# Performance work log

Measured on AMD Instinct MI355X. Metric: run time of the kernel, lower is better.

The kernel has to match this reference:

```python
import jax, jax.numpy as jnp
import numpy as np

H = 2048
NH = 16
DH = H // NH
EPS = 1e-05


def setup_inputs() -> dict:
    key = jax.random.key(0)
    ks = jax.random.split(key, 12)
    B, S, A = 4, 2048, 512
    s = 1.0 / np.sqrt(H)
    inp = {
        "hidden_states": jax.random.normal(ks[0], (B, S, H), jnp.float32),
        "audio_tokens": jax.random.normal(ks[1], (B, A, H), jnp.float32),
        "attention_mask": jax.random.randint(ks[2], (B, A), 0, 2).astype(jnp.float32),
        "Wq": jax.random.normal(ks[3], (H, H), jnp.float32) * s,
        "bq": jnp.zeros((H,), jnp.float32),
        "Wk": jax.random.normal(ks[4], (H, H), jnp.float32) * s,
        "bk": jnp.zeros((H,), jnp.float32),
        "Wv": jax.random.normal(ks[5], (H, H), jnp.float32) * s,
        "bv": jnp.zeros((H,), jnp.float32),
        "Wo": jax.random.normal(ks[6], (H, H), jnp.float32) * s,
        "bo": jnp.zeros((H,), jnp.float32),
        "gamma": jnp.ones((H,), jnp.float32),
        "beta": jnp.zeros((H,), jnp.float32),
    }
    return inp


def reference(hidden_states, audio_tokens, attention_mask,
              Wq, bq, Wk, bk, Wv, bv, Wo, bo, gamma, beta):
    B, S, _ = hidden_states.shape
    A = audio_tokens.shape[1]
    # projections (weights stored [in, out])
    q = (hidden_states @ Wq + bq).reshape(B, S, NH, DH)
    k = (audio_tokens @ Wk + bk).reshape(B, A, NH, DH)
    v = (audio_tokens @ Wv + bv).reshape(B, A, NH, DH)
    # scores: [B, NH, S, A]
    scores = jnp.einsum('bqhd,bkhd->bhqk', q, k) / np.sqrt(DH)
    scores = scores + attention_mask[:, None, None, :] * -10000.0
    probs = jax.nn.softmax(scores, axis=-1)
    # context: [B, S, NH, DH] -> [B, S, H]
    ctx = jnp.einsum('bhqk,bkhd->bqhd', probs, v).reshape(B, S, H)
    out = ctx @ Wo + bo
    # residual + LayerNorm
    x = out + hidden_states
    mu = jnp.mean(x, axis=-1, keepdims=True)
    var = jnp.mean(jnp.square(x - mu), axis=-1, keepdims=True)
    return (x - mu) * jax.lax.rsqrt(var + EPS) * gamma + beta
```

## Files before the change

### kernel.cpp

```cpp
#include <hip/hip_runtime.h>

#define HDIM 2048
#define NHEAD 16
#define DHEAD 128
#define BATCH 4
#define SEQ 2048
#define AUD 512

typedef unsigned short u16;
typedef unsigned int u32;
typedef __bf16 bf16_t;
typedef bf16_t bf16x8 __attribute__((ext_vector_type(8)));
typedef short short8 __attribute__((ext_vector_type(8)));
typedef float f32x4 __attribute__((ext_vector_type(4)));

typedef const __attribute__((address_space(1))) u32 gas_u32;
typedef __attribute__((address_space(3))) u32 las_u32;

__device__ __forceinline__ float b2f(u16 h) {
  union { u32 u; float f; } v; v.u = ((u32)h) << 16; return v.f;
}
__device__ __forceinline__ u16 f2b(float f) {
  union { float f; u32 u; } v; v.f = f;
  u32 r = (v.u + 0x7FFFu + ((v.u >> 16) & 1u)) >> 16;
  return (u16)r;
}

__global__ __launch_bounds__(256) void cvt2_k(const float* __restrict__ s0,
                                              u16* __restrict__ d0, int n0,
                                              const float* __restrict__ s1,
                                              u16* __restrict__ d1, int n1) {
  int i = blockIdx.x * 256 + threadIdx.x;
  const float* src; u16* dst; int j;
  if (i < n0) { src = s0; dst = d0; j = i; }
  else { j = i - n0; if (j >= n1) return; src = s1; dst = d1; }
  const float4* s4 = (const float4*)src;
  float4 a = s4[2 * j], b = s4[2 * j + 1];
  short8 o;
  o[0] = (short)f2b(a.x); o[1] = (short)f2b(a.y);
  o[2] = (short)f2b(a.z); o[3] = (short)f2b(a.w);
  o[4] = (short)f2b(b.x); o[5] = (short)f2b(b.y);
  o[6] = (short)f2b(b.z); o[7] = (short)f2b(b.w);
  *(short8*)(dst + (size_t)j * 8) = o;
}

__global__ __launch_bounds__(256) void transpose4_k(
    const float* __restrict__ Wq, const float* __restrict__ Wk,
    const float* __restrict__ Wv, const float* __restrict__ Wo,
    u16* __restrict__ dst4) {
  const float* src = (blockIdx.z == 0) ? Wq
                   : (blockIdx.z == 1) ? Wk
                   : (blockIdx.z == 2) ? Wv : Wo;
  u16* dst = dst4 + (size_t)blockIdx.z * HDIM * HDIM;
  __shared__ float tile[32][33];
  int tx = threadIdx.x, ty = threadIdx.y;
  int x = blockIdx.x * 32 + tx;
  int y0 = blockIdx.y * 32;
#pragma unroll
  for (int j = 0; j < 32; j += 8)
    tile[ty + j][tx] = src[(size_t)(y0 + ty + j) * HDIM + x];
  __syncthreads();
  int x2 = y0 + tx;
  int y2 = blockIdx.x * 32;
#pragma unroll
  for (int j = 0; j < 32; j += 8)
    dst[(size_t)(y2 + ty + j) * HDIM + x2] = f2b(tile[tx][ty + j]);
}

__global__ __launch_bounds__(256) void gemm_bt(
    const u16* __restrict__ A, int lda,
    const u16* __restrict__ Bt, int ldb,
    void* __restrict__ Cv, int ldc,
    const float* __restrict__ bias, float alpha, int M, int N, int K, int cmode) {
  __shared__ u16 As[128 * 32];
  __shared__ u16 Bs[128 * 32];

  int lane = threadIdx.x & 63;
  int wave = threadIdx.x >> 6;
  int gdx = gridDim.x;
  int id = blockIdx.y * gdx + blockIdx.x;
  int cpx = (gdx * gridDim.y) >> 3;
  int sid = (id & 7) * cpx + (id >> 3);
  int m0 = (sid / gdx) * 128;
  int n0 = (sid % gdx) * 128;
  int wm = (wave & 1) * 64;
  int wn = (wave >> 1) * 64;
  int row16 = lane & 15;
  int quad = lane >> 4;

  int sr = (lane >> 2);
  int sc = (lane & 3) * 8;

  f32x4 acc[4][4];
#pragma unroll
  for (int i = 0; i < 4; i++)
#pragma unroll
    for (int j = 0; j < 4; j++) acc[i][j] = (f32x4){0.f, 0.f, 0.f, 0.f};

  for (int k0 = 0; k0 < K; k0 += 32) {
#pragma unroll
    for (int t = 0; t < 2; t++) {
      int chunk = wave * 2 + t;
      int r = chunk * 16 + sr;
      const u16* ga = A + (size_t)(m0 + r) * lda + k0 + sc;
      const u16* gb = Bt + (size_t)(n0 + r) * ldb + k0 + sc;
      __builtin_amdgcn_global_load_lds((gas_u32*)ga, (las_u32*)(As + chunk * 512), 16, 0, 0);
      __builtin_amdgcn_global_load_lds((gas_u32*)gb, (las_u32*)(Bs + chunk * 512), 16, 0, 0);
    }
    __syncthreads();

    short8 af[4], bf[4];
#pragma unroll
    for (int mt = 0; mt < 4; mt++)
      af[mt] = *(const short8*)(As + (wm + mt * 16 + row16) * 32 + quad * 8);
#pragma unroll
    for (int nt = 0; nt < 4; nt++)
      bf[nt] = *(const short8*)(Bs + (wn + nt * 16 + row16) * 32 + quad * 8);
#pragma unroll
    for (int mt = 0; mt < 4; mt++)
#pragma unroll
      for (int nt = 0; nt < 4; nt++)
        acc[mt][nt] = __builtin_amdgcn_mfma_f32_16x16x32_bf16(
            __builtin_bit_cast(bf16x8, af[mt]), __builtin_bit_cast(bf16x8, bf[nt]),
            acc[mt][nt], 0, 0, 0);
    __syncthreads();
  }

#pragma unroll
  for (int nt = 0; nt < 4; nt++) {
    int nn = n0 + wn + nt * 16 + row16;
    float bv = bias ? bias[nn] : 0.f;
#pragma unroll
    for (int mt = 0; mt < 4; mt++) {
#pragma unroll
      for (int r = 0; r < 4; r++) {
        int mm = m0 + wm + mt * 16 + quad * 4 + r;
        float val = (acc[mt][nt][r] + bv) * alpha;
        if (cmode == 2) {
          ((float*)Cv)[(size_t)mm * ldc + nn] = val;
        } else if (cmode == 1) {
          int bb = mm >> 9, aa = mm & 511;
          int hh = nn >> 7, dd = nn & 127;
          ((u16*)Cv)[((size_t)((bb * 16 + hh) * 128 + dd)) * 512 + aa] = f2b(val);
        } else {
          ((u16*)Cv)[(size_t)mm * ldc + nn] = f2b(val);
        }
      }
    }
  }
}

__global__ __launch_bounds__(512, 2) void gemm_ring8(
    const u16* __restrict__ A, int lda,
    const u16* __restrict__ Bt, int ldb,
    void* __restrict__ Cv, int ldc,
    const float* __restrict__ bias, float alpha, int K, int cmode) {
  __shared__ u16 As[4][256 * 32];
  __shared__ u16 Bs[4][256 * 32];

  int tid = threadIdx.x;
  int lane = tid & 63, wave = tid >> 6;
  int wr = wave >> 2, wc = wave & 3;
  int row16 = lane & 15, quad = lane >> 4;
  int cofs = (quad * 8) ^ (((row16 >> 1) & 3) << 3);

  int gdx = gridDim.x;
  int id = blockIdx.y * gdx + blockIdx.x;
  int cpx = (gdx * gridDim.y) >> 3;
  int sid = (id & 7) * cpx + (id >> 3);
  int n0 = (sid % gdx) * 256;
  int m0 = (sid / gdx) * 256;

  int r0 = tid >> 2;
  int c0 = ((tid & 3) ^ ((r0 >> 1) & 3)) * 8;

  f32x4 acc[8][4];
#pragma unroll
  for (int i = 0; i < 8; i++)
#pragma unroll
    for (int j = 0; j < 4; j++) acc[i][j] = (f32x4){0.f, 0.f, 0.f, 0.f};

  auto stageA = [&](int slot, int k0) {
#pragma unroll
    for (int l = 0; l < 2; l++) {
      int row = l * 128 + r0;
      __builtin_amdgcn_global_load_lds(
          (gas_u32*)(A + (size_t)(m0 + row) * lda + k0 + c0),
          (las_u32*)(&As[slot][(l * 512 + tid) * 8]), 16, 0, 0);
    }
  };
  auto stageB = [&](int slot, int k0) {
#pragma unroll
    for (int l = 0; l < 2; l++) {
      int row = l * 128 + r0;
      __builtin_amdgcn_global_load_lds(
          (gas_u32*)(Bt + (size_t)(n0 + row) * ldb + k0 + c0),
          (las_u32*)(&Bs[slot][(l * 512 + tid) * 8]), 16, 0, 0);
    }
  };

  int NT = K >> 5;
  stageA(0, 0);  stageB(0, 0);
  stageA(1, 32); stageB(1, 32);
  stageA(2, 64); stageB(2, 64);
  asm volatile("s_waitcnt vmcnt(8)" ::: "memory");
  __builtin_amdgcn_s_barrier();

  for (int kt = 0; kt < NT; ++kt) {
    int slot = kt & 3;
    int sp = (kt + 3) & 3;
    bool pf = (kt + 3) < NT;
    const u16* as = &As[slot][0];
    const u16* bs = &Bs[slot][0];

    short8 bfr[4], af[4];
#pragma unroll
    for (int ni = 0; ni < 4; ni++)
      bfr[ni] = *(const short8*)(bs + (wc * 64 + ni * 16 + row16) * 32 + cofs);
#pragma unroll
    for (int mi = 0; mi < 4; mi++)
      af[mi] = *(const short8*)(as + (wr * 128 + mi * 16 + row16) * 32 + cofs);
    if (pf) stageA(sp, (kt + 3) << 5);
    __builtin_amdgcn_s_barrier();
    asm volatile("s_waitcnt lgkmcnt(0)" ::: "memory");
    __builtin_amdgcn_s_setprio(1);
#pragma unroll
    for (int mi = 0; mi < 4; mi++)
#pragma unroll
      for (int ni = 0; ni < 4; ni++)
        acc[mi][ni] = __builtin_amdgcn_mfma_f32_16x16x32_bf16(
            __builtin_bit_cast(bf16x8, af[mi]), __builtin_bit_cast(bf16x8, bfr[ni]),
            acc[mi][ni], 0, 0, 0);
    __builtin_amdgcn_s_setprio(0);
    __builtin_amdgcn_s_barrier();

    short8 ag[4];
#pragma unroll
    for (int mi = 0; mi < 4; mi++)
      ag[mi] = *(const short8*)(as + (wr * 128 + (mi + 4) * 16 + row16) * 32 + cofs);
    if (pf) stageB(sp, (kt + 3) << 5);
    {
      int nf = NT - 2 - kt;
      if (nf >= 2)      asm volatile("s_waitcnt vmcnt(8)" ::: "memory");
      else if (nf == 1) asm volatile("s_waitcnt vmcnt(4)" ::: "memory");
      else              asm volatile("s_waitcnt vmcnt(0)" ::: "memory");
    }
    __builtin_amdgcn_s_barrier();
    asm volatile("s_waitcnt lgkmcnt(0)" ::: "memory");
    __builtin_amdgcn_s_setprio(1);
#pragma unroll
    for (int mi = 0; mi < 4; mi++)
#pragma unroll
      for (int ni = 0; ni < 4; ni++)
        acc[mi + 4][ni] = __builtin_amdgcn_mfma_f32_16x16x32_bf16(
            __builtin_bit_cast(bf16x8, ag[mi]), __builtin_bit_cast(bf16x8, bfr[ni]),
            acc[mi + 4][ni], 0, 0, 0);
    __builtin_amdgcn_s_setprio(0);
    __builtin_amdgcn_s_barrier();
  }

#pragma unroll
  for (int ni = 0; ni < 4; ni++) {
    int nn = n0 + wc * 64 + ni * 16 + row16;
    float bv = bias ? bias[nn] : 0.f;
#pragma unroll
    for (int mi = 0; mi < 8; mi++) {
#pragma unroll
      for (int r = 0; r < 4; r++) {
        int mm = m0 + wr * 128 + mi * 16 + quad * 4 + r;
        float val = (acc[mi][ni][r] + bv) * alpha;
        if (cmode == 2) ((float*)Cv)[(size_t)mm * ldc + nn] = val;
        else            ((u16*)Cv)[(size_t)mm * ldc + nn] = f2b(val);
      }
    }
  }
}

__global__ __launch_bounds__(256) void flash_k(
    const u16* __restrict__ Q, const u16* __restrict__ K,
    const u16* __restrict__ Vt, const float* __restrict__ mask,
    u16* __restrict__ Ctx) {
  __shared__ u16 KP[128 * 128];
  __shared__ u16 Vs[128 * 128];

  int bh = blockIdx.y, b = bh >> 4, h = bh & 15;
  int q0 = blockIdx.x * 128;
  int lane = threadIdx.x & 63, wave = threadIdx.x >> 6;
  int row16 = lane & 15, quad = lane >> 4;
  int wq = wave * 32;
  int swr = (row16 & 7) << 3;

  const u16* qbase = Q + ((size_t)(b * SEQ + q0)) * HDIM + h * DHEAD;
  const u16* kbase = K + ((size_t)b * AUD) * HDIM + h * DHEAD;
  const u16* vbase = Vt + ((size_t)(b * NHEAD + h)) * DHEAD * AUD;
  const float* mp = mask + b * AUD;

  short8 qf[2][4];
#pragma unroll
  for (int mt = 0; mt < 2; mt++)
#pragma unroll
    for (int ks = 0; ks < 4; ks++)
      qf[mt][ks] = *(const short8*)(qbase + (size_t)(wq + mt * 16 + row16) * HDIM +
                                    ks * 32 + quad * 8);

  f32x4 oacc[2][8];
  float lacc[2][4];
#pragma unroll
  for (int mt = 0; mt < 2; mt++) {
#pragma unroll
    for (int nt = 0; nt < 8; nt++) oacc[mt][nt] = (f32x4){0.f, 0.f, 0.f, 0.f};
#pragma unroll
    for (int r = 0; r < 4; r++) lacc[mt][r] = 0.f;
  }

  int sl = (lane >> 4);
  int scol = (lane & 15) * 8;

  for (int kt = 0; kt < 4; kt++) {
#pragma unroll
    for (int t = 0; t < 8; t++) {
      int c = wave * 8 + t;
      int r = c * 4 + sl;
      int csw = scol ^ ((r & 7) << 3);
      __builtin_amdgcn_global_load_lds(
          (gas_u32*)(kbase + (size_t)(kt * 128 + r) * HDIM + csw),
          (las_u32*)(KP + c * 512), 16, 0, 0);
      __builtin_amdgcn_global_load_lds(
          (gas_u32*)(vbase + (size_t)r * AUD + kt * 128 + csw),
          (las_u32*)(Vs + c * 512), 16, 0, 0);
    }
    __syncthreads();

    f32x4 sacc[2][8];
#pragma unroll
    for (int mt = 0; mt < 2; mt++)
#pragma unroll
      for (int nt = 0; nt < 8; nt++) sacc[mt][nt] = (f32x4){0.f, 0.f, 0.f, 0.f};
#pragma unroll
    for (int ks = 0; ks < 4; ks++) {
      short8 bf[8];
      int cofs = (ks * 32 + quad * 8) ^ swr;
#pragma unroll
      for (int nt = 0; nt < 8; nt++)
        bf[nt] = *(const short8*)(KP + (nt * 16 + row16) * 128 + cofs);
      __builtin_amdgcn_s_setprio(1);
#pragma unroll
      for (int mt = 0; mt < 2; mt++)
#pragma unroll
        for (int nt = 0; nt < 8; nt++)
          sacc[mt][nt] = __builtin_amdgcn_mfma_f32_16x16x32_bf16(
              __builtin_bit_cast(bf16x8, qf[mt][ks]), __builtin_bit_cast(bf16x8, bf[nt]),
              sacc[mt][nt], 0, 0, 0);
      __builtin_amdgcn_s_setprio(0);
    }

#pragma unroll
    for (int nt = 0; nt < 8; nt++) {
      float mval = mp[kt * 128 + nt * 16 + row16] * (-10000.0f);
#pragma unroll
      for (int mt = 0; mt < 2; mt++)
#pragma unroll
        for (int r = 0; r < 4; r++) {
          float e = __expf(sacc[mt][nt][r] + mval);
          sacc[mt][nt][r] = e;
          lacc[mt][r] += e;
        }
    }
    __syncthreads();

#pragma unroll
    for (int mt = 0; mt < 2; mt++)
#pragma unroll
      for (int nt = 0; nt < 8; nt++)
#pragma unroll
        for (int r = 0; r < 4; r++) {
          int prow = wq + mt * 16 + quad * 4 + r;
          KP[prow * 128 + ((nt * 16 + row16) ^ ((prow & 7) << 3))] =
              f2b(sacc[mt][nt][r]);
        }
    __syncthreads();

#pragma unroll
    for (int ks = 0; ks < 4; ks++) {
      short8 af[2], bf[8];
      int cofs = (ks * 32 + quad * 8) ^ swr;
#pragma unroll
      for (int mt = 0; mt < 2; mt++)
        af[mt] = *(const short8*)(KP + (wq + mt * 16 + row16) * 128 + cofs);
#pragma unroll
      for (int nt = 0; nt < 8; nt++)
        bf[nt] = *(const short8*)(Vs + (nt * 16 + row16) * 128 + cofs);
      __builtin_amdgcn_s_setprio(1);
#pragma unroll
      for (int mt = 0; mt < 2; mt++)
#pragma unroll
        for (int nt = 0; nt < 8; nt++)
          oacc[mt][nt] = __builtin_amdgcn_mfma_f32_16x16x32_bf16(
              __builtin_bit_cast(bf16x8, af[mt]), __builtin_bit_cast(bf16x8, bf[nt]),
              oacc[mt][nt], 0, 0, 0);
      __builtin_amdgcn_s_setprio(0);
    }
    __syncthreads();
  }

#pragma unroll
  for (int mt = 0; mt < 2; mt++)
#pragma unroll
    for (int r = 0; r < 4; r++) {
      float s = lacc[mt][r];
      for (int off = 1; off < 16; off <<= 1) s += __shfl_xor(s, off, 64);
      lacc[mt][r] = 1.0f / s;
    }

  u16* cb = Ctx + ((size_t)(b * SEQ + q0 + wq)) * HDIM + h * DHEAD;
#pragma unroll
  for (int mt = 0; mt < 2; mt++)
#pragma unroll
    for (int nt = 0; nt < 8; nt++)
#pragma unroll
      for (int r = 0; r < 4; r++)
        cb[(size_t)(mt * 16 + quad * 4 + r) * HDIM + nt * 16 + row16] =
            f2b(oacc[mt][nt][r] * lacc[mt][r]);
}

__global__ __launch_bounds__(256) void ln_k(const float* O,
                                            const float* __restrict__ hs,
                                            const float* __restrict__ gamma,
                                            const float* __restrict__ beta,
                                            float* out) {
  size_t rowoff = (size_t)blockIdx.x * HDIM;
  float x[8], sum = 0.f, sq = 0.f;
#pragma unroll
  for (int i = 0; i < 8; i++) {
    int idx = threadIdx.x + 256 * i;
    float v = O[rowoff + idx] + hs[rowoff + idx];
    x[i] = v;
    sum += v;
    sq += v * v;
  }
  for (int off = 32; off; off >>= 1) {
    sum += __shfl_xor(sum, off, 64);
    sq += __shfl_xor(sq, off, 64);
  }
  __shared__ float red[8];
  int wave = threadIdx.x >> 6, lane = threadIdx.x & 63;
  if (lane == 0) { red[wave] = sum; red[4 + wave] = sq; }
  __syncthreads();
  sum = red[0] + red[1] + red[2] + red[3];
  sq = red[4] + red[5] + red[6] + red[7];
  float mu = sum * (1.0f / HDIM);
  float var = sq * (1.0f / HDIM) - mu * mu;
  float inv = rsqrtf(var + 1e-5f);
#pragma unroll
  for (int i = 0; i < 8; i++) {
    int idx = threadIdx.x + 256 * i;
    out[rowoff + idx] = (x[i] - mu) * inv * gamma[idx] + beta[idx];
  }
}

extern "C" void kernel_launch(void* const* d_in, const int* in_sizes, int n_in,
                              void* d_out, int out_size, void* d_ws, size_t ws_size,
                              hipStream_t stream) {
  (void)in_sizes; (void)n_in; (void)out_size; (void)ws_size;
  const float* hs   = (const float*)d_in[0];
  const float* at   = (const float*)d_in[1];
  const float* mask = (const float*)d_in[2];
  const float* Wq = (const float*)d_in[3];  const float* bq = (const float*)d_in[4];
  const float* Wk = (const float*)d_in[5];  const float* bk = (const float*)d_in[6];
  const float* Wv = (const float*)d_in[7];  const float* bv = (const float*)d_in[8];
  const float* Wo = (const float*)d_in[9];  const float* bo = (const float*)d_in[10];
  const float* gamma = (const float*)d_in[11];
  const float* beta  = (const float*)d_in[12];
  float* out = (float*)d_out;
  u16* ws = (u16*)d_ws;

  u16* hsb = ws;
  u16* atb = ws + 16777216;
  u16* wT4 = ws + 20971520;
  u16* Q   = ws + 37748736;
  u16* Kb  = ws + 54525952;
  u16* Vt  = ws + 58720256;
  u16* Ctx = ws + 62914560;
  u16* wTq = wT4;
  u16* wTk = wT4 + 4194304;
  u16* wTv = wT4 + 8388608;
  u16* wTo = wT4 + 12582912;

  cvt2_k<<<10240, 256, 0, stream>>>(hs, hsb, 2097152, at, atb, 524288);
  transpose4_k<<<dim3(64, 64, 4), dim3(32, 8), 0, stream>>>(Wq, Wk, Wv, Wo, wT4);

  const float qscale = 0.08838834764831845f;

  gemm_ring8<<<dim3(8, 32), 512, 0, stream>>>(hsb, HDIM, wTq, HDIM, Q, HDIM,
                                              bq, qscale, 2048, 0);
  gemm_bt<<<dim3(16, 16), 256, 0, stream>>>(atb, HDIM, wTk, HDIM, Kb, HDIM,
                                            bk, 1.0f, 2048, 2048, 2048, 0);
  gemm_bt<<<dim3(16, 16), 256, 0, stream>>>(atb, HDIM, wTv, HDIM, Vt, HDIM,
                                            bv, 1.0f, 2048, 2048, 2048, 1);

  flash_k<<<dim3(SEQ / 128, BATCH * NHEAD), 256, 0, stream>>>(Q, Kb, Vt, mask, Ctx);

  gemm_ring8<<<dim3(8, 32), 512, 0, stream>>>(Ctx, HDIM, wTo, HDIM, out, HDIM,
                                              bo, 1.0f, 2048, 2);
  ln_k<<<8192, 256, 0, stream>>>(out, hs, gamma, beta, out);
}
```

Measured before the change: 594.4 us.

## Prefetch next K/V tile into registers during the PV MFMA phase

The first K/V tile is now loaded into LDS before the loop. Each later tile is read from global memory into registers while the P·V MFMAs run, then written into the swizzled LDS buffers after a barrier, which hides global-load latency behind compute. `__syncthreads` is replaced by explicit lgkmcnt waits plus `s_barrier`, and the `s_setprio` hints around the MFMA blocks are removed. The trade-off is 64 extra VGPRs per lane for the prefetch buffers, which may lower occupancy, and the prefetched K/V data now takes a register round trip instead of a direct global-to-LDS load.

```diff
diff --git a/kernel.cpp b/kernel.cpp
--- a/kernel.cpp
+++ b/kernel.cpp
@@ -316,21 +316,21 @@
   int sl = (lane >> 4);
   int scol = (lane & 15) * 8;
 
+#pragma unroll
+  for (int t = 0; t < 8; t++) {
+    int c = wave * 8 + t;
+    int r = c * 4 + sl;
+    int csw = scol ^ ((r & 7) << 3);
+    __builtin_amdgcn_global_load_lds(
+        (gas_u32*)(kbase + (size_t)r * HDIM + csw),
+        (las_u32*)(KP + c * 512), 16, 0, 0);
+    __builtin_amdgcn_global_load_lds(
+        (gas_u32*)(vbase + (size_t)r * AUD + csw),
+        (las_u32*)(Vs + c * 512), 16, 0, 0);
+  }
+  __syncthreads();
+
   for (int kt = 0; kt < 4; kt++) {
-#pragma unroll
-    for (int t = 0; t < 8; t++) {
-      int c = wave * 8 + t;
-      int r = c * 4 + sl;
-      int csw = scol ^ ((r & 7) << 3);
-      __builtin_amdgcn_global_load_lds(
-          (gas_u32*)(kbase + (size_t)(kt * 128 + r) * HDIM + csw),
-          (las_u32*)(KP + c * 512), 16, 0, 0);
-      __builtin_amdgcn_global_load_lds(
-          (gas_u32*)(vbase + (size_t)r * AUD + kt * 128 + csw),
-          (las_u32*)(Vs + c * 512), 16, 0, 0);
-    }
-    __syncthreads();
-
     f32x4 sacc[2][8];
 #pragma unroll
     for (int mt = 0; mt < 2; mt++)
@@ -343,7 +343,6 @@
 #pragma unroll
       for (int nt = 0; nt < 8; nt++)
         bf[nt] = *(const short8*)(KP + (nt * 16 + row16) * 128 + cofs);
-      __builtin_amdgcn_s_setprio(1);
 #pragma unroll
       for (int mt = 0; mt < 2; mt++)
 #pragma unroll
@@ -351,7 +350,6 @@
           sacc[mt][nt] = __builtin_amdgcn_mfma_f32_16x16x32_bf16(
               __builtin_bit_cast(bf16x8, qf[mt][ks]), __builtin_bit_cast(bf16x8, bf[nt]),
               sacc[mt][nt], 0, 0, 0);
-      __builtin_amdgcn_s_setprio(0);
     }
 
 #pragma unroll
@@ -366,7 +364,9 @@
           lacc[mt][r] += e;
         }
     }
-    __syncthreads();
+
+    asm volatile("s_waitcnt lgkmcnt(0)" ::: "memory");
+    __builtin_amdgcn_s_barrier();
 
 #pragma unroll
     for (int mt = 0; mt < 2; mt++)
@@ -378,7 +378,16 @@
           KP[prow * 128 + ((nt * 16 + row16) ^ ((prow & 7) << 3))] =
               f2b(sacc[mt][nt][r]);
         }
-    __syncthreads();
+
+    short8 kreg[8], vreg[8];
+    if (kt < 3) {
+#pragma unroll
+      for (int t = 0; t < 8; t++) {
+        int r = wq + t * 4 + sl;
+        kreg[t] = *(const short8*)(kbase + (size_t)((kt + 1) * 128 + r) * HDIM + scol);
+        vreg[t] = *(const short8*)(vbase + (size_t)r * AUD + (kt + 1) * 128 + scol);
+      }
+    }
 
 #pragma unroll
     for (int ks = 0; ks < 4; ks++) {
@@ -390,7 +399,6 @@
 #pragma unroll
       for (int nt = 0; nt < 8; nt++)
         bf[nt] = *(const short8*)(Vs + (nt * 16 + row16) * 128 + cofs);
-      __builtin_amdgcn_s_setprio(1);
 #pragma unroll
       for (int mt = 0; mt < 2; mt++)
 #pragma unroll
@@ -398,9 +406,23 @@
           oacc[mt][nt] = __builtin_amdgcn_mfma_f32_16x16x32_bf16(
               __builtin_bit_cast(bf16x8, af[mt]), __builtin_bit_cast(bf16x8, bf[nt]),
               oacc[mt][nt], 0, 0, 0);
-      __builtin_amdgcn_s_setprio(0);
-    }
-    __syncthreads();
+    }
+
+    asm volatile("s_waitcnt lgkmcnt(0)" ::: "memory");
+    __builtin_amdgcn_s_barrier();
+
+    if (kt < 3) {
+      asm volatile("s_waitcnt vmcnt(0)" ::: "memory");
+#pragma unroll
+      for (int t = 0; t < 8; t++) {
+        int r = wq + t * 4 + sl;
+        int cs = scol ^ ((r & 7) << 3);
+        *(short8*)(KP + r * 128 + cs) = kreg[t];
+        *(short8*)(Vs + r * 128 + cs) = vreg[t];
+      }
+    }
+    asm volatile("s_waitcnt lgkmcnt(0)" ::: "memory");
+    __builtin_amdgcn_s_barrier();
   }
 
 #pragma unroll
```

Result: no change. 594.0 us (-0.1%).
